# Performance work log

Measured on AMD Instinct MI355X. Metric: run time of the kernel, lower is better.

The kernel has to match this reference:

```python
import jax, jax.numpy as jnp
import numpy as np

H = 8        # hidden_size
T = 609      # seq_size
IN = 5       # input feature dim
B = 2048     # batch


def _lstm_layer(x, Wih, Whh, bih, bhh):
    """PyTorch-compatible single-layer LSTM, batch_first. x: [B, T, I].
    Gate order i, f, g, o; zero initial (h, c)."""
    b = x.shape[0]
    h_dim = Wih.shape[0] // 4
    bias = bih + bhh

    def step(carry, xt):
        h, c = carry
        gates = xt @ Wih.T + h @ Whh.T + bias          # [B, 4H]
        i, f, g, o = jnp.split(gates, 4, axis=-1)
        i = jax.nn.sigmoid(i)
        f = jax.nn.sigmoid(f)
        g = jnp.tanh(g)
        o = jax.nn.sigmoid(o)
        c = f * c + i * g
        h = o * jnp.tanh(c)
        return (h, c), h

    h0 = jnp.zeros((b, h_dim), x.dtype)
    (_, _), ys = jax.lax.scan(step, (h0, h0), jnp.swapaxes(x, 0, 1))  # ys: [T, B, H]
    return jnp.swapaxes(ys, 0, 1)                                      # [B, T, H]


def setup_inputs() -> dict:
    key = jax.random.key(0)
    ks = jax.random.split(key, 20)
    s_lstm = 1.0 / np.sqrt(H)   # PyTorch LSTM init scale

    def u(k, shape, s):
        return jax.random.uniform(k, shape, jnp.float32, -s, s)

    inp = {"x": jax.random.normal(ks[0], (B, T, IN), jnp.float32)}
    # LSTM layer 1 (input 5), layers 2-3 (input H)
    ins = [IN, H, H]
    for l in range(3):
        k0, k1, k2, k3 = jax.random.split(ks[1 + l], 4)
        inp[f"Wih{l+1}"] = u(k0, (4 * H, ins[l]), s_lstm)
        inp[f"Whh{l+1}"] = u(k1, (4 * H, H), s_lstm)
        inp[f"bih{l+1}"] = u(k2, (4 * H,), s_lstm)
        inp[f"bhh{l+1}"] = u(k3, (4 * H,), s_lstm)
    # MLP head
    d_in = H * T  # 4872
    dims = [(4096, d_in), (1024, 4096), (T, 1024)]
    for i, (o, ii) in enumerate(dims):
        s = 1.0 / np.sqrt(ii)
        k0, k1 = jax.random.split(ks[10 + i], 2)
        inp[f"W{i+1}"] = u(k0, (o, ii), s)
        inp[f"b{i+1}"] = u(k1, (o,), s)
    return inp


def reference(x, Wih1, Whh1, bih1, bhh1, Wih2, Whh2, bih2, bhh2,
              Wih3, Whh3, bih3, bhh3, W1, b1, W2, b2, W3, b3):
    out = _lstm_layer(x, Wih1, Whh1, bih1, bhh1)
    out = _lstm_layer(out, Wih2, Whh2, bih2, bhh2)
    out = _lstm_layer(out, Wih3, Whh3, bih3, bhh3)
    out = out.reshape(x.shape[0], -1)              # [B, T*H]
    out = jax.nn.relu(out @ W1.T + b1)
    out = jax.nn.relu(out @ W2.T + b2)
    out = out @ W3.T + b3                          # [B, T]
    return out
```

## Files before the change

### kernel.cpp

```cpp
#include <hip/hip_runtime.h>
#include <hip/hip_bf16.h>

typedef __attribute__((ext_vector_type(8))) short short8;
typedef __attribute__((ext_vector_type(4))) float floatx4;
typedef __attribute__((ext_vector_type(2))) float f32x2;
typedef __attribute__((ext_vector_type(2))) int i32x2;
typedef unsigned short u16;

#define T_SZ 609
#define K1V  4872
#define K1P  4896
#define RD   16

static __device__ __forceinline__ u16 f2bf(float f) {
    union { float f; unsigned u; } a; a.f = f;
    unsigned r = a.u + 0x7FFF + ((a.u >> 16) & 1);
    return (u16)(r >> 16);
}

static __device__ __forceinline__ void gload_lds16(const u16* g, u16* l) {
    __builtin_amdgcn_global_load_lds(
        (const __attribute__((address_space(1))) void*)g,
        (__attribute__((address_space(3))) void*)l, 16, 0, 0);
}

#define WG_LOAD(p)     __hip_atomic_load((p), __ATOMIC_ACQUIRE, __HIP_MEMORY_SCOPE_WORKGROUP)
#define WG_STORE(p, v) __hip_atomic_store((p), (v), __ATOMIC_RELEASE, __HIP_MEMORY_SCOPE_WORKGROUP)

template<int CTRL>
static __device__ __forceinline__ float dppf(float v) {
    union { float f; int i; } a, b;
    a.f = v;
    b.i = __builtin_amdgcn_update_dpp(0, a.i, CTRL, 0xF, 0xF, true);
    return b.f;
}

static __device__ __forceinline__ void pl16(float v, float& ev, float& od) {
    union { float f; int i; } a; a.f = v;
    i32x2 r = __builtin_amdgcn_permlane16_swap(a.i, a.i, false, false);
    union { int i; float f; } x, y; x.i = r.x; y.i = r.y;
    ev = x.f; od = y.f;
}

static __device__ __forceinline__ void bfly2(float v, f32x2* o) {
    o[0] = (f32x2){v,              dppf<0xB1>(v)};
    o[1] = (f32x2){dppf<0x4E>(v),  dppf<0x1B>(v)};
    float m7 = dppf<0x141>(v);
    o[2] = (f32x2){dppf<0x1B>(m7), dppf<0x4E>(m7)};
    o[3] = (f32x2){dppf<0xB1>(m7), m7};
}

static __device__ __forceinline__ float tns(float a) {
    return __builtin_fmaf(2.f, __fdividef(1.f, 1.f + __expf(-2.f * a)), -1.f);
}

static __device__ __forceinline__ void cvt8(const float* __restrict__ p, u16* __restrict__ d) {
    float4 a = *(const float4*)p;
    float4 b = *(const float4*)(p + 4);
    u16 o[8] = { f2bf(a.x), f2bf(a.y), f2bf(a.z), f2bf(a.w),
                 f2bf(b.x), f2bf(b.y), f2bf(b.z), f2bf(b.w) };
    *(uint4*)d = *(const uint4*)o;
}
static __device__ __forceinline__ void zero8(u16* __restrict__ d) {
    *(uint4*)d = (uint4){0, 0, 0, 0};
}

__global__ __launch_bounds__(192) void lstm3_fused(
    const float* __restrict__ x,
    const float* __restrict__ Wih1, const float* __restrict__ Whh1,
    const float* __restrict__ bih1, const float* __restrict__ bhh1,
    const float* __restrict__ Wih2, const float* __restrict__ Whh2,
    const float* __restrict__ bih2, const float* __restrict__ bhh2,
    const float* __restrict__ Wih3, const float* __restrict__ Whh3,
    const float* __restrict__ bih3, const float* __restrict__ bhh3,
    u16* __restrict__ A1,
    const float* __restrict__ W1, u16* __restrict__ W1b,
    const float* __restrict__ W2, u16* __restrict__ W2b,
    const float* __restrict__ W3, u16* __restrict__ W3b)
{
    if (blockIdx.x >= 1024) {
        const int ct = (blockIdx.x - 1024) * 192 + threadIdx.x;
        const int cs = 256 * 192;
        for (int i = ct; i < 4096 * 612; i += cs) {
            int r = i / 612, c = (i - r * 612) << 3;
            u16* d = W1b + (size_t)r * K1P + c;
            if (c < K1V) cvt8(W1 + (size_t)r * K1V + c, d); else zero8(d);
        }
        for (int i = ct; i < 524288; i += cs)
            cvt8(W2 + (size_t)i * 8, W2b + (size_t)i * 8);
        for (int i = ct; i < 640 * 128; i += cs) {
            int r = i >> 7, c = (i & 127) << 3;
            u16* d = W3b + (size_t)r * 1024 + c;
            if (r < T_SZ) cvt8(W3 + (size_t)r * 1024 + c, d); else zero8(d);
        }
        return;
    }

    __shared__ __align__(16) float xs[2 * T_SZ * 5];
    __shared__ __align__(16) float r1[RD * 16], r2[RD * 16];
    __shared__ int p1, p2, c2, c3;

    const int tid = threadIdx.x;
    const int b0  = blockIdx.x * 2;

    const float* xg = x + (size_t)b0 * (T_SZ * 5);
    for (int i = tid; i < 2 * T_SZ * 5; i += 192) xs[i] = xg[i];
    if (tid == 0) { p1 = 0; p2 = 0; c2 = 0; c3 = 0; }
    if (tid < 48) {
        int rr = tid / 24, cc = tid - rr * 24;
        A1[(size_t)(b0 + rr) * K1P + K1V + cc] = 0;
    }
    __syncthreads();

    const int lane = tid & 63, wid = tid >> 6;
    const int rh   = lane >> 5;
    const int gj   = lane & 31;
    const int grp  = gj >> 3;
    const int j    = gj & 7;
    const int ptg  = (grp == 1) ? 2 : ((grp == 2) ? 1 : grp);
    const int G    = ptg * 8 + j;

    const float am = (grp == 1) ? -2.f : -1.f;
    const float aa = (grp == 1) ?  2.f :  1.f;
    const float ab = (grp == 1) ? -1.f :  0.f;
    const bool  isf = (grp == 2);

    auto lfin = [&](float a, float cin, float& cout) -> float {
        float e   = __expf(am * a);
        float v   = __builtin_fmaf(aa, __fdividef(1.f, 1.f + e), ab);
        float w1_ = dppf<0x128>(v);
        float ig  = v * w1_;
        float fv  = isf ? v : w1_;
        float m   = (lane & 16) ? fv : ig;
        float igA, ffA; pl16(m, igA, ffA);
        float cn  = __builtin_fmaf(ffA, cin, igA);
        cout = cn;
        float th  = tns(cn);
        float ov  = isf ? w1_ : v;
        float h   = ov * th;
        float he, ho; pl16(h, he, ho);
        return ho;
    };

    if (wid == 0) {
        float wi5[5]; f32x2 whbf[4];
#pragma unroll
        for (int k = 0; k < 5; ++k) wi5[k] = Wih1[G * 5 + k];
#pragma unroll
        for (int m = 0; m < 4; ++m) {
            int ka = j ^ (2 * m), kb = ka ^ 1;
            whbf[m] = (f32x2){Whh1[G * 8 + ka], Whh1[G * 8 + kb]};
        }
        const float bs = bih1[G] + bhh1[G];
        const float* xr = &xs[rh * (T_SZ * 5)];
        float xc[5];
#pragma unroll
        for (int k = 0; k < 5; ++k) xc[k] = xr[k];
        float h1r = 0.f, c1s = 0.f;
#pragma unroll 1
        for (int t = 0; t < T_SZ; ++t) {
            if ((t & 3) == 0) while (WG_LOAD(&c2) < t - 8) {}
            float a = bs;
#pragma unroll
            for (int k = 0; k < 5; ++k) a = __builtin_fmaf(wi5[k], xc[k], a);
            f32x2 u[4]; bfly2(h1r, u);
            f32x2 B = (f32x2){0.f, 0.f};
#pragma unroll
            for (int m = 0; m < 4; ++m) B = __builtin_elementwise_fma(whbf[m], u[m], B);
            a += B.x + B.y;
            float cn; float hn = lfin(a, c1s, cn); c1s = cn; h1r = hn;
            if (grp == 0) r1[(t & (RD - 1)) * 16 + rh * 8 + j] = hn;
            if (lane == 0 && (((t & 3) == 3) || t == T_SZ - 1)) WG_STORE(&p1, t + 1);
            int tn = (t + 1 < T_SZ) ? t + 1 : T_SZ - 1;
#pragma unroll
            for (int k = 0; k < 5; ++k) xc[k] = xr[tn * 5 + k];
        }
    } else if (wid == 1) {
        f32x2 win[4], whbf[4];
#pragma unroll
        for (int m = 0; m < 4; ++m) {
            int ka = j ^ (2 * m), kb = ka ^ 1;
            win[m]  = (f32x2){Wih2[G * 8 + 2 * m], Wih2[G * 8 + 2 * m + 1]};
            whbf[m] = (f32x2){Whh2[G * 8 + ka],    Whh2[G * 8 + kb]};
        }
        const float bs = bih2[G] + bhh2[G];
        while (WG_LOAD(&p1) < 4) {}
        f32x2 hp[4];
        { const f32x2* s = (const f32x2*)&r1[rh * 8];
          hp[0] = s[0]; hp[1] = s[1]; hp[2] = s[2]; hp[3] = s[3]; }
        float h2r = 0.f, c2s = 0.f;
#pragma unroll 1
        for (int t = 0; t < T_SZ; ++t) {
            if ((t & 3) == 0 && t) {
                int need = (t + 4 < T_SZ) ? t + 4 : T_SZ;
                while (WG_LOAD(&p1) < need) {}
                while (WG_LOAD(&c3) < t - 8) {}
                const f32x2* s = (const f32x2*)&r1[(t & (RD - 1)) * 16 + rh * 8];
                hp[0] = s[0]; hp[1] = s[1]; hp[2] = s[2]; hp[3] = s[3];
            }
            f32x2 A = (f32x2){bs, 0.f};
#pragma unroll
            for (int m = 0; m < 4; ++m) A = __builtin_elementwise_fma(win[m], hp[m], A);
            f32x2 u[4]; bfly2(h2r, u);
            f32x2 B = (f32x2){0.f, 0.f};
#pragma unroll
            for (int m = 0; m < 4; ++m) B = __builtin_elementwise_fma(whbf[m], u[m], B);
            float a = A.x + A.y + B.x + B.y;
            float cn; float hn = lfin(a, c2s, cn); c2s = cn; h2r = hn;
            if (grp == 0) r2[(t & (RD - 1)) * 16 + rh * 8 + j] = hn;
            if (lane == 0 && (((t & 3) == 3) || t == T_SZ - 1)) {
                WG_STORE(&c2, t + 1);
                WG_STORE(&p2, t + 1);
            }
            if ((t & 3) != 3) {
                const f32x2* s = (const f32x2*)&r1[((t + 1) & (RD - 1)) * 16 + rh * 8];
                hp[0] = s[0]; hp[1] = s[1]; hp[2] = s[2]; hp[3] = s[3];
            }
        }
    } else {
        f32x2 win[4], whbf[4];
#pragma unroll
        for (int m = 0; m < 4; ++m) {
            int ka = j ^ (2 * m), kb = ka ^ 1;
            win[m]  = (f32x2){Wih3[G * 8 + 2 * m], Wih3[G * 8 + 2 * m + 1]};
            whbf[m] = (f32x2){Whh3[G * 8 + ka],    Whh3[G * 8 + kb]};
        }
        const float bs = bih3[G] + bhh3[G];
        u16* outp = A1 + (size_t)(b0 + rh) * K1P;
        while (WG_LOAD(&p2) < 4) {}
        f32x2 hp[4];
        { const f32x2* s = (const f32x2*)&r2[rh * 8];
          hp[0] = s[0]; hp[1] = s[1]; hp[2] = s[2]; hp[3] = s[3]; }
        float h3r = 0.f, c3s = 0.f;
#pragma unroll 1
        for (int t = 0; t < T_SZ; ++t) {
            if ((t & 3) == 0 && t) {
                int need = (t + 4 < T_SZ) ? t + 4 : T_SZ;
                while (WG_LOAD(&p2) < need) {}
                const f32x2* s = (const f32x2*)&r2[(t & (RD - 1)) * 16 + rh * 8];
                hp[0] = s[0]; hp[1] = s[1]; hp[2] = s[2]; hp[3] = s[3];
            }
            f32x2 A = (f32x2){bs, 0.f};
#pragma unroll
            for (int m = 0; m < 4; ++m) A = __builtin_elementwise_fma(win[m], hp[m], A);
            f32x2 u[4]; bfly2(h3r, u);
            f32x2 B = (f32x2){0.f, 0.f};
#pragma unroll
            for (int m = 0; m < 4; ++m) B = __builtin_elementwise_fma(whbf[m], u[m], B);
            float a = A.x + A.y + B.x + B.y;
            float cn; float hn = lfin(a, c3s, cn); c3s = cn; h3r = hn;
            if (grp == 0) outp[t * 8 + j] = f2bf(hn);
            if (lane == 0 && (((t & 3) == 3) || t == T_SZ - 1)) WG_STORE(&c3, t + 1);
            if ((t & 3) != 3) {
                const f32x2* s = (const f32x2*)&r2[((t + 1) & (RD - 1)) * 16 + rh * 8];
                hp[0] = s[0]; hp[1] = s[1]; hp[2] = s[2]; hp[3] = s[3];
            }
        }
    }
}

template<int BM, int BN, bool RELU, bool NGUARD, bool OUTF32>
__global__ __launch_bounds__(256) void gemm_bt(
    const u16* __restrict__ A, int lda,
    const u16* __restrict__ B, int ldb,
    const float* __restrict__ bias,
    void* __restrict__ Cv, int ldc, int N, int K)
{
    constexpr int WM = BM / 2, WN = BN / 2;
    constexpr int TM = WM / 16, TN = WN / 16;
    __shared__ u16 As[BM * 32];
    __shared__ u16 Bs[BN * 32];

    const int tid = threadIdx.x;
    const int bm  = blockIdx.y * BM;
    const int bn  = blockIdx.x * BN;
    const int l   = tid & 63, w = tid >> 6;
    const int wr  = w >> 1, wc = w & 1;
    const int lr  = l & 15, q = l >> 4;
    const int lrow = l >> 2;
    const int lcol = (l & 3) << 3;

    floatx4 acc[TM][TN];
#pragma unroll
    for (int i = 0; i < TM; ++i)
#pragma unroll
        for (int j = 0; j < TN; ++j) acc[i][j] = (floatx4){0.f, 0.f, 0.f, 0.f};

    const u16* Ab = A + (size_t)bm * lda;
    const u16* Bb = B + (size_t)bn * ldb;

    for (int k0 = 0; k0 < K; k0 += 32) {
#pragma unroll
        for (int i = 0; i < BM / 64; ++i) {
            int r0 = w * (BM / 4) + i * 16;
            gload_lds16(Ab + (size_t)(r0 + lrow) * lda + k0 + lcol, &As[r0 * 32]);
        }
#pragma unroll
        for (int i = 0; i < BN / 64; ++i) {
            int r0 = w * (BN / 4) + i * 16;
            gload_lds16(Bb + (size_t)(r0 + lrow) * ldb + k0 + lcol, &Bs[r0 * 32]);
        }
        __syncthreads();

        short8 fa[TM], fb[TN];
#pragma unroll
        for (int i = 0; i < TM; ++i)
            fa[i] = *(const short8*)&As[(wr * WM + i * 16 + lr) * 32 + q * 8];
#pragma unroll
        for (int j = 0; j < TN; ++j)
            fb[j] = *(const short8*)&Bs[(wc * WN + j * 16 + lr) * 32 + q * 8];
#pragma unroll
        for (int i = 0; i < TM; ++i)
#pragma unroll
            for (int j = 0; j < TN; ++j)
                acc[i][j] = __builtin_amdgcn_mfma_f32_16x16x32_bf16(fa[i], fb[j], acc[i][j], 0, 0, 0);
        __syncthreads();
    }

#pragma unroll
    for (int j = 0; j < TN; ++j) {
        int n = bn + wc * WN + j * 16 + lr;
        bool nok = (!NGUARD) || (n < N);
        float bv = nok ? bias[n] : 0.f;
#pragma unroll
        for (int i = 0; i < TM; ++i) {
            int m0r = bm + wr * WM + i * 16 + q * 4;
#pragma unroll
            for (int r = 0; r < 4; ++r) {
                float vv = acc[i][j][r] + bv;
                if (RELU) vv = fmaxf(vv, 0.f);
                if (nok) {
                    size_t idx = (size_t)(m0r + r) * ldc + n;
                    if (OUTF32) ((float*)Cv)[idx] = vv;
                    else        ((u16*)Cv)[idx] = f2bf(vv);
                }
            }
        }
    }
}

extern "C" void kernel_launch(void* const* d_in, const int* in_sizes, int n_in,
                              void* d_out, int out_size, void* d_ws, size_t ws_size,
                              hipStream_t stream)
{
    const float* x    = (const float*)d_in[0];
    const float* Wih1 = (const float*)d_in[1];
    const float* Whh1 = (const float*)d_in[2];
    const float* bih1 = (const float*)d_in[3];
    const float* bhh1 = (const float*)d_in[4];
    const float* Wih2 = (const float*)d_in[5];
    const float* Whh2 = (const float*)d_in[6];
    const float* bih2 = (const float*)d_in[7];
    const float* bhh2 = (const float*)d_in[8];
    const float* Wih3 = (const float*)d_in[9];
    const float* Whh3 = (const float*)d_in[10];
    const float* bih3 = (const float*)d_in[11];
    const float* bhh3 = (const float*)d_in[12];
    const float* W1 = (const float*)d_in[13];
    const float* b1 = (const float*)d_in[14];
    const float* W2 = (const float*)d_in[15];
    const float* b2 = (const float*)d_in[16];
    const float* W3 = (const float*)d_in[17];
    const float* b3 = (const float*)d_in[18];

    u16* A1  = (u16*)d_ws;
    u16* A2  = A1  + (size_t)2048 * K1P;
    u16* A3  = A2  + (size_t)2048 * 4096;
    u16* W1b = A3  + (size_t)2048 * 1024;
    u16* W2b = W1b + (size_t)4096 * K1P;
    u16* W3b = W2b + (size_t)1024 * 4096;

    lstm3_fused<<<1280, 192, 0, stream>>>(x, Wih1, Whh1, bih1, bhh1,
                                          Wih2, Whh2, bih2, bhh2,
                                          Wih3, Whh3, bih3, bhh3, A1,
                                          W1, W1b, W2, W2b, W3, W3b);

    gemm_bt<128, 128, true, false, false><<<dim3(32, 16), 256, 0, stream>>>(
        A1, K1P, W1b, K1P, b1, A2, 4096, 4096, K1P);

    gemm_bt<64, 128, true, false, false><<<dim3(8, 32), 256, 0, stream>>>(
        A2, 4096, W2b, 4096, b2, A3, 1024, 1024, 4096);

    gemm_bt<64, 128, false, true, true><<<dim3(5, 32), 256, 0, stream>>>(
        A3, 1024, W3b, 1024, b3, d_out, T_SZ, T_SZ, 1024);
}
```

Before: 684.9 us.

## Unroll LSTM time loop by four and compute input projection via DPP exchange

Each of the three LSTM warps now runs its time loop in blocks of four steps with a peeled last step. Instead of every lane reading all previous-layer h values (or all 5 x features) from LDS, each lane loads only its own element and uses DPP lane shuffles to form the input dot product, as the recurrent term already does. Inputs for the next four steps are prefetched one block ahead, and flag polling and stores happen once per block rather than being checked every step. This trades many LDS reads and per-step branches for extra DPP moves and scalar FMAs, and it relies on the consumer waiting for t0+8 so that the prefetched ring slots are ready.

```diff
diff --git a/kernel.cpp b/kernel.cpp
--- a/kernel.cpp
+++ b/kernel.cpp
@@ -3,7 +3,6 @@
 
 typedef __attribute__((ext_vector_type(8))) short short8;
 typedef __attribute__((ext_vector_type(4))) float floatx4;
-typedef __attribute__((ext_vector_type(2))) float f32x2;
 typedef __attribute__((ext_vector_type(2))) int i32x2;
 typedef unsigned short u16;
 
@@ -42,12 +41,17 @@
     ev = x.f; od = y.f;
 }
 
-static __device__ __forceinline__ void bfly2(float v, f32x2* o) {
-    o[0] = (f32x2){v,              dppf<0xB1>(v)};
-    o[1] = (f32x2){dppf<0x4E>(v),  dppf<0x1B>(v)};
-    float m7 = dppf<0x141>(v);
-    o[2] = (f32x2){dppf<0x1B>(m7), dppf<0x4E>(m7)};
-    o[3] = (f32x2){dppf<0xB1>(m7), m7};
+static __device__ __forceinline__ float dotx(const float* w, float h, float acc) {
+    acc = __builtin_fmaf(w[0], h, acc);
+    acc = __builtin_fmaf(w[1], dppf<0xB1>(h), acc);
+    acc = __builtin_fmaf(w[2], dppf<0x4E>(h), acc);
+    acc = __builtin_fmaf(w[3], dppf<0x1B>(h), acc);
+    float m7 = dppf<0x141>(h);
+    acc = __builtin_fmaf(w[7], m7, acc);
+    acc = __builtin_fmaf(w[6], dppf<0xB1>(m7), acc);
+    acc = __builtin_fmaf(w[5], dppf<0x4E>(m7), acc);
+    acc = __builtin_fmaf(w[4], dppf<0x1B>(m7), acc);
+    return acc;
 }
 
 static __device__ __forceinline__ float tns(float a) {
@@ -142,119 +146,122 @@
         return ho;
     };
 
+    const int rj = rh * 8 + j;
+
     if (wid == 0) {
-        float wi5[5]; f32x2 whbf[4];
-#pragma unroll
-        for (int k = 0; k < 5; ++k) wi5[k] = Wih1[G * 5 + k];
-#pragma unroll
-        for (int m = 0; m < 4; ++m) {
-            int ka = j ^ (2 * m), kb = ka ^ 1;
-            whbf[m] = (f32x2){Whh1[G * 8 + ka], Whh1[G * 8 + kb]};
+        float wiv[8], whv[8];
+#pragma unroll
+        for (int m = 0; m < 8; ++m) {
+            int k = j ^ m;
+            wiv[m] = (k < 5) ? Wih1[G * 5 + k] : 0.f;
+            whv[m] = Whh1[G * 8 + k];
         }
         const float bs = bih1[G] + bhh1[G];
+        const int jx = (j < 5) ? j : 0;
         const float* xr = &xs[rh * (T_SZ * 5)];
-        float xc[5];
-#pragma unroll
-        for (int k = 0; k < 5; ++k) xc[k] = xr[k];
+        float xc4[4], xn4[4];
+#pragma unroll
+        for (int q = 0; q < 4; ++q) xc4[q] = xr[q * 5 + jx];
         float h1r = 0.f, c1s = 0.f;
 #pragma unroll 1
-        for (int t = 0; t < T_SZ; ++t) {
-            if ((t & 3) == 0) while (WG_LOAD(&c2) < t - 8) {}
-            float a = bs;
-#pragma unroll
-            for (int k = 0; k < 5; ++k) a = __builtin_fmaf(wi5[k], xc[k], a);
-            f32x2 u[4]; bfly2(h1r, u);
-            f32x2 B = (f32x2){0.f, 0.f};
-#pragma unroll
-            for (int m = 0; m < 4; ++m) B = __builtin_elementwise_fma(whbf[m], u[m], B);
-            a += B.x + B.y;
-            float cn; float hn = lfin(a, c1s, cn); c1s = cn; h1r = hn;
-            if (grp == 0) r1[(t & (RD - 1)) * 16 + rh * 8 + j] = hn;
-            if (lane == 0 && (((t & 3) == 3) || t == T_SZ - 1)) WG_STORE(&p1, t + 1);
-            int tn = (t + 1 < T_SZ) ? t + 1 : T_SZ - 1;
-#pragma unroll
-            for (int k = 0; k < 5; ++k) xc[k] = xr[tn * 5 + k];
+        for (int t0 = 0; t0 < 608; t0 += 4) {
+            while (WG_LOAD(&c2) < t0 - 8) {}
+            const float* xp = xr + (t0 + 4) * 5 + jx;
+            xn4[0] = xp[0]; xn4[1] = xp[5]; xn4[2] = xp[10]; xn4[3] = xp[15];
+            const int sb = (t0 & 15);
+#pragma unroll
+            for (int q = 0; q < 4; ++q) {
+                float a = dotx(wiv, xc4[q], bs);
+                float b = dotx(whv, h1r, 0.f);
+                float cn; float hv = lfin(a + b, c1s, cn); c1s = cn; h1r = hv;
+                if (grp == 0) r1[(sb + q) * 16 + rj] = hv;
+            }
+            if (lane == 0) WG_STORE(&p1, t0 + 4);
+            xc4[0] = xn4[0]; xc4[1] = xn4[1]; xc4[2] = xn4[2]; xc4[3] = xn4[3];
+        }
+        {
+            float a = dotx(wiv, xc4[0], bs);
+            float b = dotx(whv, h1r, 0.f);
+            float cn; float hv = lfin(a + b, c1s, cn);
+            if (grp == 0) r1[0 * 16 + rj] = hv;
+            if (lane == 0) WG_STORE(&p1, 609);
         }
     } else if (wid == 1) {
-        f32x2 win[4], whbf[4];
-#pragma unroll
-        for (int m = 0; m < 4; ++m) {
-            int ka = j ^ (2 * m), kb = ka ^ 1;
-            win[m]  = (f32x2){Wih2[G * 8 + 2 * m], Wih2[G * 8 + 2 * m + 1]};
-            whbf[m] = (f32x2){Whh2[G * 8 + ka],    Whh2[G * 8 + kb]};
+        float win[8], whn[8];
+#pragma unroll
+        for (int m = 0; m < 8; ++m) {
+            int k = j ^ m;
+            win[m] = Wih2[G * 8 + k];
+            whn[m] = Whh2[G * 8 + k];
         }
         const float bs = bih2[G] + bhh2[G];
         while (WG_LOAD(&p1) < 4) {}
-        f32x2 hp[4];
-        { const f32x2* s = (const f32x2*)&r1[rh * 8];
-          hp[0] = s[0]; hp[1] = s[1]; hp[2] = s[2]; hp[3] = s[3]; }
+        float hc[4], hn[4];
+        hc[0] = r1[0 * 16 + rj]; hc[1] = r1[1 * 16 + rj];
+        hc[2] = r1[2 * 16 + rj]; hc[3] = r1[3 * 16 + rj];
         float h2r = 0.f, c2s = 0.f;
 #pragma unroll 1
-        for (int t = 0; t < T_SZ; ++t) {
-            if ((t & 3) == 0 && t) {
-                int need = (t + 4 < T_SZ) ? t + 4 : T_SZ;
-                while (WG_LOAD(&p1) < need) {}
-                while (WG_LOAD(&c3) < t - 8) {}
-                const f32x2* s = (const f32x2*)&r1[(t & (RD - 1)) * 16 + rh * 8];
-                hp[0] = s[0]; hp[1] = s[1]; hp[2] = s[2]; hp[3] = s[3];
+        for (int t0 = 0; t0 < 608; t0 += 4) {
+            int pt = (t0 + 8 <= 609) ? t0 + 8 : 609;
+            while (WG_LOAD(&p1) < pt) {}
+            while (WG_LOAD(&c3) < t0 - 8) {}
+            const float* s = &r1[((t0 + 4) & 15) * 16 + rj];
+            hn[0] = s[0]; hn[1] = s[16]; hn[2] = s[32]; hn[3] = s[48];
+            const int sb = (t0 & 15);
+#pragma unroll
+            for (int q = 0; q < 4; ++q) {
+                float a = dotx(win, hc[q], bs);
+                float b = dotx(whn, h2r, 0.f);
+                float cn; float hv = lfin(a + b, c2s, cn); c2s = cn; h2r = hv;
+                if (grp == 0) r2[(sb + q) * 16 + rj] = hv;
             }
-            f32x2 A = (f32x2){bs, 0.f};
-#pragma unroll
-            for (int m = 0; m < 4; ++m) A = __builtin_elementwise_fma(win[m], hp[m], A);
-            f32x2 u[4]; bfly2(h2r, u);
-            f32x2 B = (f32x2){0.f, 0.f};
-#pragma unroll
-            for (int m = 0; m < 4; ++m) B = __builtin_elementwise_fma(whbf[m], u[m], B);
-            float a = A.x + A.y + B.x + B.y;
-            float cn; float hn = lfin(a, c2s, cn); c2s = cn; h2r = hn;
-            if (grp == 0) r2[(t & (RD - 1)) * 16 + rh * 8 + j] = hn;
-            if (lane == 0 && (((t & 3) == 3) || t == T_SZ - 1)) {
-                WG_STORE(&c2, t + 1);
-                WG_STORE(&p2, t + 1);
-            }
-            if ((t & 3) != 3) {
-                const f32x2* s = (const f32x2*)&r1[((t + 1) & (RD - 1)) * 16 + rh * 8];
-                hp[0] = s[0]; hp[1] = s[1]; hp[2] = s[2]; hp[3] = s[3];
-            }
+            if (lane == 0) { WG_STORE(&c2, t0 + 4); WG_STORE(&p2, t0 + 4); }
+            hc[0] = hn[0]; hc[1] = hn[1]; hc[2] = hn[2]; hc[3] = hn[3];
+        }
+        {
+            float a = dotx(win, hc[0], bs);
+            float b = dotx(whn, h2r, 0.f);
+            float cn; float hv = lfin(a + b, c2s, cn);
+            if (grp == 0) r2[0 * 16 + rj] = hv;
+            if (lane == 0) { WG_STORE(&c2, 609); WG_STORE(&p2, 609); }
         }
     } else {
-        f32x2 win[4], whbf[4];
-#pragma unroll
-        for (int m = 0; m < 4; ++m) {
-            int ka = j ^ (2 * m), kb = ka ^ 1;
-            win[m]  = (f32x2){Wih3[G * 8 + 2 * m], Wih3[G * 8 + 2 * m + 1]};
-            whbf[m] = (f32x2){Whh3[G * 8 + ka],    Whh3[G * 8 + kb]};
+        float win[8], whn[8];
+#pragma unroll
+        for (int m = 0; m < 8; ++m) {
+            int k = j ^ m;
+            win[m] = Wih3[G * 8 + k];
+            whn[m] = Whh3[G * 8 + k];
         }
         const float bs = bih3[G] + bhh3[G];
         u16* outp = A1 + (size_t)(b0 + rh) * K1P;
         while (WG_LOAD(&p2) < 4) {}
-        f32x2 hp[4];
-        { const f32x2* s = (const f32x2*)&r2[rh * 8];
-          hp[0] = s[0]; hp[1] = s[1]; hp[2] = s[2]; hp[3] = s[3]; }
+        float hc[4], hn[4];
+        hc[0] = r2[0 * 16 + rj]; hc[1] = r2[1 * 16 + rj];
+        hc[2] = r2[2 * 16 + rj]; hc[3] = r2[3 * 16 + rj];
         float h3r = 0.f, c3s = 0.f;
 #pragma unroll 1
-        for (int t = 0; t < T_SZ; ++t) {
-            if ((t & 3) == 0 && t) {
-                int need = (t + 4 < T_SZ) ? t + 4 : T_SZ;
-                while (WG_LOAD(&p2) < need) {}
-                const f32x2* s = (const f32x2*)&r2[(t & (RD - 1)) * 16 + rh * 8];
-                hp[0] = s[0]; hp[1] = s[1]; hp[2] = s[2]; hp[3] = s[3];
+        for (int t0 = 0; t0 < 608; t0 += 4) {
+            int pt = (t0 + 8 <= 609) ? t0 + 8 : 609;
+            while (WG_LOAD(&p2) < pt) {}
+            const float* s = &r2[((t0 + 4) & 15) * 16 + rj];
+            hn[0] = s[0]; hn[1] = s[16]; hn[2] = s[32]; hn[3] = s[48];
+#pragma unroll
+            for (int q = 0; q < 4; ++q) {
+                float a = dotx(win, hc[q], bs);
+                float b = dotx(whn, h3r, 0.f);
+                float cn; float hv = lfin(a + b, c3s, cn); c3s = cn; h3r = hv;
+                if (grp == 0) outp[(t0 + q) * 8 + j] = f2bf(hv);
             }
-            f32x2 A = (f32x2){bs, 0.f};
-#pragma unroll
-            for (int m = 0; m < 4; ++m) A = __builtin_elementwise_fma(win[m], hp[m], A);
-            f32x2 u[4]; bfly2(h3r, u);
-            f32x2 B = (f32x2){0.f, 0.f};
-#pragma unroll
-            for (int m = 0; m < 4; ++m) B = __builtin_elementwise_fma(whbf[m], u[m], B);
-            float a = A.x + A.y + B.x + B.y;
-            float cn; float hn = lfin(a, c3s, cn); c3s = cn; h3r = hn;
-            if (grp == 0) outp[t * 8 + j] = f2bf(hn);
-            if (lane == 0 && (((t & 3) == 3) || t == T_SZ - 1)) WG_STORE(&c3, t + 1);
-            if ((t & 3) != 3) {
-                const f32x2* s = (const f32x2*)&r2[((t + 1) & (RD - 1)) * 16 + rh * 8];
-                hp[0] = s[0]; hp[1] = s[1]; hp[2] = s[2]; hp[3] = s[3];
-            }
+            if (lane == 0) WG_STORE(&c3, t0 + 4);
+            hc[0] = hn[0]; hc[1] = hn[1]; hc[2] = hn[2]; hc[3] = hn[3];
+        }
+        {
+            float a = dotx(win, hc[0], bs);
+            float b = dotx(whn, h3r, 0.f);
+            float cn; float hv = lfin(a + b, c3s, cn);
+            if (grp == 0) outp[608 * 8 + j] = f2bf(hv);
+            if (lane == 0) WG_STORE(&c3, 609);
         }
     }
 }
```

Result: no change. 695.8 us (+1.6%).
